# Kernel optimization log

Hardware: AMD Instinct MI355X
Metric: run time of the kernel (lower is better)

## Reference

```python
import jax, jax.numpy as jnp
import numpy as np

D, H, W, C = 24, 24, 16, 2        # image_dims + num_classes
THETA_ALPHA = 160.0               # bilateral spatial std
THETA_BETA = 3.0                  # bilateral intensity std
THETA_GAMMA = 3.0                 # spatial-only std
NUM_ITERATIONS = 5
N = D * H * W


def _gauss_kernel(feats):
    # Dense Gaussian kernel K_ij = exp(-0.5 * ||f_i - f_j||^2).
    # This is the exact filter that the permutohedral lattice approximates
    # (self-term included, matching the lattice splat/blur/slice behaviour).
    sq = jnp.sum(feats * feats, axis=-1)               # [N]
    d2 = sq[:, None] + sq[None, :] - 2.0 * feats @ feats.T
    return jnp.exp(-0.5 * jnp.maximum(d2, 0.0))        # [N, N]


def _positions():
    zz, yy, xx = jnp.meshgrid(jnp.arange(D), jnp.arange(H), jnp.arange(W), indexing='ij')
    return jnp.stack([zz, yy, xx], axis=-1).reshape(N, 3).astype(jnp.float32)


def setup_inputs() -> dict:
    key = jax.random.key(0)
    k1, k2 = jax.random.split(key)
    unaries = jax.random.normal(k1, (1, D, H, W, C), dtype=jnp.float32)
    rgb = jax.random.uniform(k2, (1, D, H, W, 1), dtype=jnp.float32)
    # learned params (build() initial values)
    spatial_ker_weights = jnp.array([1.41, 1.41], dtype=jnp.float32)
    bilateral_ker_weights = jnp.array([3.85, 3.85], dtype=jnp.float32)
    compatibility_matrix = jnp.eye(C, dtype=jnp.float32)
    return dict(unaries=unaries, rgb=rgb,
                spatial_ker_weights=spatial_ker_weights,
                bilateral_ker_weights=bilateral_ker_weights,
                compatibility_matrix=compatibility_matrix)


def reference(unaries, rgb, spatial_ker_weights, bilateral_ker_weights, compatibility_matrix):
    out_shape = unaries.shape
    u = unaries.reshape(N, C)                 # batch index 0 only, as in the TF code
    img = rgb.reshape(N, -1)
    pos = _positions()

    Ks = _gauss_kernel(pos / THETA_GAMMA)                                        # spatial kernel [N,N]
    Kb = _gauss_kernel(jnp.concatenate([pos / THETA_ALPHA, img / THETA_BETA], -1))  # bilateral kernel [N,N]

    # normalization = filter applied to all-ones (row sums)
    norm_s = jnp.sum(Ks, axis=-1, keepdims=True)   # [N,1]
    norm_b = jnp.sum(Kb, axis=-1, keepdims=True)   # [N,1]

    q = u
    for _ in range(NUM_ITERATIONS):
        spatial_out = (Ks @ q) / norm_s            # [N,C]
        bilateral_out = (Kb @ q) / norm_b          # [N,C]
        # diag(w_s) @ spatial.T + diag(w_b) @ bilateral.T  ==  per-class scaling
        message = spatial_out * spatial_ker_weights + bilateral_out * bilateral_ker_weights
        pairwise = message @ compatibility_matrix.T  # (compat @ msg.T).T
        q = u - pairwise
    return q.reshape(out_shape)
```

## Files before the change

kernel.cpp:

```cpp
#include <hip/hip_runtime.h>


#define DD 24
#define HH 24
#define WW 16
#define SLICE 384
#define NPTS 9216
#define NT 5
#define NFI 12
#define NFT 17
#define LOG2E 1.4426950408889634f
#define K3L   (LOG2E / 18.0f)
#define K160L (LOG2E / 51200.0f)

static __device__ __forceinline__ int iabs(int a) { return a < 0 ? -a : a; }

__global__ __launch_bounds__(SLICE)
void k_xy(const float2* __restrict__ qsrc, const float* __restrict__ rgb,
          float* __restrict__ tmp) {
    __shared__ float gk[32];
    __shared__ float sA[HH][WW + 1];
    __shared__ float sB[HH][WW + 1];
    const int z = blockIdx.x, f = blockIdx.y, t = threadIdx.x;
    const int y = t >> 4, x = t & 15;
    const int i = z * SLICE + t;

    const float kk = (f < 2) ? K3L : K160L;
    if (t < DD) gk[t] = exp2f(-(float)(t * t) * kk);

    float v;
    if (f < 2) {
        float2 q = qsrc[i];
        v = (f == 0) ? q.x : q.y;
    } else {
        float I3 = rgb[i] * (1.f / 3.f);
        float E = exp2f(-0.5f * LOG2E * I3 * I3);
        int k = (f < NFI) ? ((f - 2) >> 1) : (f - NFI);
        float P = E;
        for (int s = 0; s < k; ++s) P *= I3;
        if (f < NFI) {
            float2 q = qsrc[i];
            v = P * (((f - 2) & 1) ? q.y : q.x);
        } else {
            v = P;
        }
    }
    sA[y][x] = v;
    __syncthreads();

    float a = 0.f;
#pragma unroll
    for (int xp = 0; xp < WW; ++xp) a = fmaf(gk[iabs(x - xp)], sA[y][xp], a);
    sB[y][x] = a;
    __syncthreads();

    float b = 0.f;
#pragma unroll
    for (int yp = 0; yp < HH; ++yp) b = fmaf(gk[iabs(y - yp)], sB[yp][x], b);
    tmp[f * NPTS + i] = b;
}

__global__ __launch_bounds__(SLICE)
void k_zconv(const float* __restrict__ tmp, float* __restrict__ zout) {
    __shared__ float gk[32];
    const int z = blockIdx.x, f = blockIdx.y, t = threadIdx.x;
    const float kk = (f < 2) ? K3L : K160L;
    if (t < DD) gk[t] = exp2f(-(float)(t * t) * kk);
    __syncthreads();

    float acc = 0.f;
    const float* p = tmp + f * NPTS + t;
#pragma unroll 4
    for (int zp = 0; zp < DD; ++zp)
        acc = fmaf(gk[iabs(z - zp)], p[zp * SLICE], acc);
    zout[f * NPTS + z * SLICE + t] = acc;
}

__global__ __launch_bounds__(256)
void k_update(const float* __restrict__ zout, const float* __restrict__ rgb,
              const float2* __restrict__ u2,
              const float* __restrict__ sw, const float* __restrict__ bw,
              const float* __restrict__ compat,
              float* __restrict__ normb, float2* __restrict__ qnew,
              float2* __restrict__ out, int it) {
    __shared__ float g3s[32];
    const int t = threadIdx.x;
    const int i = blockIdx.x * 256 + t;
    if (t < DD) g3s[t] = exp2f(-(float)(t * t) * K3L);
    __syncthreads();

    const int z = i / SLICE;
    const int yx = i - z * SLICE;
    const int y = yx >> 4, x = yx & 15;

    float sx = 0.f, sy = 0.f, sz = 0.f;
#pragma unroll
    for (int xp = 0; xp < WW; ++xp) sx += g3s[iabs(x - xp)];
#pragma unroll
    for (int yp = 0; yp < HH; ++yp) sy += g3s[iabs(y - yp)];
#pragma unroll
    for (int zp = 0; zp < DD; ++zp) sz += g3s[iabs(z - zp)];
    const float inv_ns = 1.0f / (sx * sy * sz);

    const float I3 = rgb[i] * (1.f / 3.f);
    const float E = exp2f(-0.5f * LOG2E * I3 * I3);
    float Pt[NT];
    Pt[0] = E;
#pragma unroll
    for (int k = 1; k < NT; ++k) Pt[k] = Pt[k - 1] * I3;
    const float invf[NT] = {1.f, 1.f, 0.5f, 1.f / 6.f, 1.f / 24.f};

    float inv_nb;
    if (it == 0) {
        float nb = 0.f;
#pragma unroll
        for (int k = 0; k < NT; ++k)
            nb = fmaf(Pt[k] * invf[k], zout[(NFI + k) * NPTS + i], nb);
        normb[i] = nb;
        inv_nb = 1.0f / nb;
    } else {
        inv_nb = 1.0f / normb[i];
    }

    float b0 = 0.f, b1 = 0.f;
#pragma unroll
    for (int k = 0; k < NT; ++k) {
        float w = Pt[k] * invf[k];
        b0 = fmaf(w, zout[(2 + 2 * k) * NPTS + i], b0);
        b1 = fmaf(w, zout[(3 + 2 * k) * NPTS + i], b1);
    }
    b0 *= inv_nb;
    b1 *= inv_nb;

    float s0 = zout[i] * inv_ns;
    float s1 = zout[NPTS + i] * inv_ns;

    float m0 = s0 * sw[0] + b0 * bw[0];
    float m1 = s1 * sw[1] + b1 * bw[1];
    float p0 = fmaf(compat[0], m0, compat[1] * m1);
    float p1 = fmaf(compat[2], m0, compat[3] * m1);
    const float2 uu = u2[i];
    float2 qn = make_float2(uu.x - p0, uu.y - p1);
    qnew[i] = qn;
    if (it == 4) out[i] = qn;
}

extern "C" void kernel_launch(void* const* d_in, const int* in_sizes, int n_in,
                              void* d_out, int out_size, void* d_ws, size_t ws_size,
                              hipStream_t stream) {
    const float2* u2     = (const float2*)d_in[0];
    const float*  rgb    = (const float*)d_in[1];
    const float*  sw     = (const float*)d_in[2];
    const float*  bw     = (const float*)d_in[3];
    const float*  compat = (const float*)d_in[4];
    float2* out = (float2*)d_out;

    float* ws = (float*)d_ws;
    float*  tmp   = ws;
    float*  zout  = ws + NFT * NPTS;
    float*  normb = ws + 2 * NFT * NPTS;
    float2* qnew  = (float2*)(ws + 2 * NFT * NPTS + NPTS);

    k_xy<<<dim3(DD, NFT), SLICE, 0, stream>>>(u2, rgb, tmp);

    for (int it = 0; it < 5; ++it) {
        k_zconv<<<dim3(DD, it == 0 ? NFT : NFI), SLICE, 0, stream>>>(tmp, zout);
        k_update<<<NPTS / 256, 256, 0, stream>>>(zout, rgb, u2, sw, bw, compat,
                                                 normb, qnew, out, it);
        if (it < 4)
            k_xy<<<dim3(DD, NFI), SLICE, 0, stream>>>((const float2*)qnew, rgb, tmp);
    }
}
```

Baseline: 109.4 us.

## Fuse z-convolution, mean-field update and next xy-filter into one iteration kernel

After: 272.6 us. 149% more time.

```diff
diff --git a/kernel.cpp b/kernel.cpp
--- a/kernel.cpp
+++ b/kernel.cpp
@@ -16,8 +16,8 @@
 static __device__ __forceinline__ int iabs(int a) { return a < 0 ? -a : a; }
 
 __global__ __launch_bounds__(SLICE)
-void k_xy(const float2* __restrict__ qsrc, const float* __restrict__ rgb,
-          float* __restrict__ tmp) {
+void k_pre(const float2* __restrict__ u2, const float* __restrict__ rgb,
+           float* __restrict__ tmpA, float* __restrict__ tmpN) {
     __shared__ float gk[32];
     __shared__ float sA[HH][WW + 1];
     __shared__ float sB[HH][WW + 1];
@@ -30,7 +30,7 @@
 
     float v;
     if (f < 2) {
-        float2 q = qsrc[i];
+        float2 q = u2[i];
         v = (f == 0) ? q.x : q.y;
     } else {
         float I3 = rgb[i] * (1.f / 3.f);
@@ -39,7 +39,7 @@
         float P = E;
         for (int s = 0; s < k; ++s) P *= I3;
         if (f < NFI) {
-            float2 q = qsrc[i];
+            float2 q = u2[i];
             v = P * (((f - 2) & 1) ? q.y : q.x);
         } else {
             v = P;
@@ -57,42 +57,16 @@
     float b = 0.f;
 #pragma unroll
     for (int yp = 0; yp < HH; ++yp) b = fmaf(gk[iabs(y - yp)], sB[yp][x], b);
-    tmp[f * NPTS + i] = b;
-}
-
-__global__ __launch_bounds__(SLICE)
-void k_zconv(const float* __restrict__ tmp, float* __restrict__ zout) {
-    __shared__ float gk[32];
-    const int z = blockIdx.x, f = blockIdx.y, t = threadIdx.x;
-    const float kk = (f < 2) ? K3L : K160L;
-    if (t < DD) gk[t] = exp2f(-(float)(t * t) * kk);
-    __syncthreads();
-
-    float acc = 0.f;
-    const float* p = tmp + f * NPTS + t;
-#pragma unroll 4
-    for (int zp = 0; zp < DD; ++zp)
-        acc = fmaf(gk[iabs(z - zp)], p[zp * SLICE], acc);
-    zout[f * NPTS + z * SLICE + t] = acc;
-}
-
-__global__ __launch_bounds__(256)
-void k_update(const float* __restrict__ zout, const float* __restrict__ rgb,
-              const float2* __restrict__ u2,
-              const float* __restrict__ sw, const float* __restrict__ bw,
-              const float* __restrict__ compat,
-              float* __restrict__ normb, float2* __restrict__ qnew,
-              float2* __restrict__ out, int it) {
-    __shared__ float g3s[32];
-    const int t = threadIdx.x;
-    const int i = blockIdx.x * 256 + t;
-    if (t < DD) g3s[t] = exp2f(-(float)(t * t) * K3L);
-    __syncthreads();
-
-    const int z = i / SLICE;
-    const int yx = i - z * SLICE;
-    const int y = yx >> 4, x = yx & 15;
-
+    float* dst = (f < NFI) ? (tmpA + f * NPTS) : (tmpN + (f - NFI) * NPTS);
+    dst[i] = b;
+}
+
+static __device__ __forceinline__ void mf_update(
+        const float acc[12], const float* g3s, const float* Pt,
+        float inv_nb, int y, int x, int z,
+        const float* sw, const float* bw, const float* compat,
+        const float2 uu, float* q0o, float* q1o) {
+    const float invf[NT] = {1.f, 1.f, 0.5f, 1.f / 6.f, 1.f / 24.f};
     float sx = 0.f, sy = 0.f, sz = 0.f;
 #pragma unroll
     for (int xp = 0; xp < WW; ++xp) sx += g3s[iabs(x - xp)];
@@ -101,6 +75,60 @@
 #pragma unroll
     for (int zp = 0; zp < DD; ++zp) sz += g3s[iabs(z - zp)];
     const float inv_ns = 1.0f / (sx * sy * sz);
+
+    float b0 = 0.f, b1 = 0.f;
+#pragma unroll
+    for (int k = 0; k < NT; ++k) {
+        float w = Pt[k] * invf[k];
+        b0 = fmaf(w, acc[2 + 2 * k], b0);
+        b1 = fmaf(w, acc[3 + 2 * k], b1);
+    }
+    b0 *= inv_nb;
+    b1 *= inv_nb;
+    float s0 = acc[0] * inv_ns;
+    float s1 = acc[1] * inv_ns;
+    float m0 = s0 * sw[0] + b0 * bw[0];
+    float m1 = s1 * sw[1] + b1 * bw[1];
+    float p0 = fmaf(compat[0], m0, compat[1] * m1);
+    float p1 = fmaf(compat[2], m0, compat[3] * m1);
+    *q0o = uu.x - p0;
+    *q1o = uu.y - p1;
+}
+
+__global__ __launch_bounds__(SLICE)
+void k_iter(const float* __restrict__ tsrc, float* __restrict__ tdst,
+            const float* __restrict__ tmpN, const float* __restrict__ rgb,
+            const float2* __restrict__ u2,
+            const float* __restrict__ sw, const float* __restrict__ bw,
+            const float* __restrict__ compat,
+            float* __restrict__ normb, int it) {
+    __shared__ float g3s[32];
+    __shared__ float g160s[32];
+    __shared__ float2 cA[HH][WW + 1];
+    __shared__ float2 cB[HH][WW + 1];
+    const int z = blockIdx.x, g = blockIdx.y, t = threadIdx.x;
+    const int y = t >> 4, x = t & 15;
+    const int i = z * SLICE + t;
+
+    if (t < DD) {
+        g3s[t] = exp2f(-(float)(t * t) * K3L);
+        g160s[t] = exp2f(-(float)(t * t) * K160L);
+    }
+    __syncthreads();
+
+    float acc[12];
+#pragma unroll
+    for (int f = 0; f < 12; ++f) acc[f] = 0.f;
+    for (int zp = 0; zp < DD; ++zp) {
+        int d = iabs(z - zp);
+        float w3 = g3s[d], wb = g160s[d];
+        const float* base = tsrc + zp * SLICE + t;
+        acc[0] = fmaf(w3, base[0], acc[0]);
+        acc[1] = fmaf(w3, base[NPTS], acc[1]);
+#pragma unroll
+        for (int f = 2; f < 12; ++f)
+            acc[f] = fmaf(wb, base[f * NPTS], acc[f]);
+    }
 
     const float I3 = rgb[i] * (1.f / 3.f);
     const float E = exp2f(-0.5f * LOG2E * I3 * I3);
@@ -108,41 +136,105 @@
     Pt[0] = E;
 #pragma unroll
     for (int k = 1; k < NT; ++k) Pt[k] = Pt[k - 1] * I3;
-    const float invf[NT] = {1.f, 1.f, 0.5f, 1.f / 6.f, 1.f / 24.f};
 
     float inv_nb;
     if (it == 0) {
+        const float invf[NT] = {1.f, 1.f, 0.5f, 1.f / 6.f, 1.f / 24.f};
+        float accN[NT] = {0.f, 0.f, 0.f, 0.f, 0.f};
+        for (int zp = 0; zp < DD; ++zp) {
+            float wb = g160s[iabs(z - zp)];
+            const float* base = tmpN + zp * SLICE + t;
+#pragma unroll
+            for (int k = 0; k < NT; ++k)
+                accN[k] = fmaf(wb, base[k * NPTS], accN[k]);
+        }
         float nb = 0.f;
 #pragma unroll
-        for (int k = 0; k < NT; ++k)
-            nb = fmaf(Pt[k] * invf[k], zout[(NFI + k) * NPTS + i], nb);
-        normb[i] = nb;
+        for (int k = 0; k < NT; ++k) nb = fmaf(Pt[k] * invf[k], accN[k], nb);
+        if (g == 0) normb[i] = nb;
         inv_nb = 1.0f / nb;
     } else {
         inv_nb = 1.0f / normb[i];
     }
 
+    float q0, q1;
+    mf_update(acc, g3s, Pt, inv_nb, y, x, z, sw, bw, compat, u2[i], &q0, &q1);
+
+    float2 v;
+    const float* gk;
+    if (g == 0) { v = make_float2(q0, q1); gk = g3s; }
+    else        { float P = Pt[g - 1]; v = make_float2(P * q0, P * q1); gk = g160s; }
+
+    cA[y][x] = v;
+    __syncthreads();
+    float a0 = 0.f, a1 = 0.f;
+#pragma unroll
+    for (int xp = 0; xp < WW; ++xp) {
+        float w = gk[iabs(x - xp)];
+        float2 vv = cA[y][xp];
+        a0 = fmaf(w, vv.x, a0);
+        a1 = fmaf(w, vv.y, a1);
+    }
+    cB[y][x] = make_float2(a0, a1);
+    __syncthreads();
     float b0 = 0.f, b1 = 0.f;
 #pragma unroll
-    for (int k = 0; k < NT; ++k) {
-        float w = Pt[k] * invf[k];
-        b0 = fmaf(w, zout[(2 + 2 * k) * NPTS + i], b0);
-        b1 = fmaf(w, zout[(3 + 2 * k) * NPTS + i], b1);
-    }
-    b0 *= inv_nb;
-    b1 *= inv_nb;
-
-    float s0 = zout[i] * inv_ns;
-    float s1 = zout[NPTS + i] * inv_ns;
-
-    float m0 = s0 * sw[0] + b0 * bw[0];
-    float m1 = s1 * sw[1] + b1 * bw[1];
-    float p0 = fmaf(compat[0], m0, compat[1] * m1);
-    float p1 = fmaf(compat[2], m0, compat[3] * m1);
-    const float2 uu = u2[i];
-    float2 qn = make_float2(uu.x - p0, uu.y - p1);
-    qnew[i] = qn;
-    if (it == 4) out[i] = qn;
+    for (int yp = 0; yp < HH; ++yp) {
+        float w = gk[iabs(y - yp)];
+        float2 vv = cB[yp][x];
+        b0 = fmaf(w, vv.x, b0);
+        b1 = fmaf(w, vv.y, b1);
+    }
+    tdst[(2 * g) * NPTS + i] = b0;
+    tdst[(2 * g + 1) * NPTS + i] = b1;
+}
+
+__global__ __launch_bounds__(128)
+void k_final(const float* __restrict__ tsrc, const float* __restrict__ rgb,
+             const float2* __restrict__ u2,
+             const float* __restrict__ sw, const float* __restrict__ bw,
+             const float* __restrict__ compat,
+             const float* __restrict__ normb, float2* __restrict__ out) {
+    __shared__ float g3s[32];
+    __shared__ float g160s[32];
+    const int t = threadIdx.x;
+    const int i = blockIdx.x * 128 + t;
+    const int z = i / SLICE;
+    const int yx = i - z * SLICE;
+    const int y = yx >> 4, x = yx & 15;
+    const int col = yx;
+
+    if (t < DD) {
+        g3s[t] = exp2f(-(float)(t * t) * K3L);
+        g160s[t] = exp2f(-(float)(t * t) * K160L);
+    }
+    __syncthreads();
+
+    float acc[12];
+#pragma unroll
+    for (int f = 0; f < 12; ++f) acc[f] = 0.f;
+    for (int zp = 0; zp < DD; ++zp) {
+        int d = iabs(z - zp);
+        float w3 = g3s[d], wb = g160s[d];
+        const float* base = tsrc + zp * SLICE + col;
+        acc[0] = fmaf(w3, base[0], acc[0]);
+        acc[1] = fmaf(w3, base[NPTS], acc[1]);
+#pragma unroll
+        for (int f = 2; f < 12; ++f)
+            acc[f] = fmaf(wb, base[f * NPTS], acc[f]);
+    }
+
+    const float I3 = rgb[i] * (1.f / 3.f);
+    const float E = exp2f(-0.5f * LOG2E * I3 * I3);
+    float Pt[NT];
+    Pt[0] = E;
+#pragma unroll
+    for (int k = 1; k < NT; ++k) Pt[k] = Pt[k - 1] * I3;
+
+    float q0, q1;
+    mf_update(acc, g3s, Pt, 1.0f / normb[i], y, x, z, sw, bw, compat,
+              u2[i], &q0, &q1);
+    out[i] = make_float2(q0, q1);
 }
 
 extern "C" void kernel_launch(void* const* d_in, const int* in_sizes, int n_in,
@@ -156,18 +248,22 @@
     float2* out = (float2*)d_out;
 
     float* ws = (float*)d_ws;
-    float*  tmp   = ws;
-    float*  zout  = ws + NFT * NPTS;
-    float*  normb = ws + 2 * NFT * NPTS;
-    float2* qnew  = (float2*)(ws + 2 * NFT * NPTS + NPTS);
-
-    k_xy<<<dim3(DD, NFT), SLICE, 0, stream>>>(u2, rgb, tmp);
-
-    for (int it = 0; it < 5; ++it) {
-        k_zconv<<<dim3(DD, it == 0 ? NFT : NFI), SLICE, 0, stream>>>(tmp, zout);
-        k_update<<<NPTS / 256, 256, 0, stream>>>(zout, rgb, u2, sw, bw, compat,
-                                                 normb, qnew, out, it);
-        if (it < 4)
-            k_xy<<<dim3(DD, NFI), SLICE, 0, stream>>>((const float2*)qnew, rgb, tmp);
-    }
-}
+    float* tmpA  = ws;
+    float* tmpB  = ws + NFI * NPTS;
+    float* tmpN  = ws + 2 * NFI * NPTS;
+    float* normb = ws + (2 * NFI + NT) * NPTS;
+
+    k_pre<<<dim3(DD, NFT), SLICE, 0, stream>>>(u2, rgb, tmpA, tmpN);
+
+    const float* tsrc = tmpA;
+    float* tdst = tmpB;
+    for (int it = 0; it < 4; ++it) {
+        k_iter<<<dim3(DD, 6), SLICE, 0, stream>>>(tsrc, tdst, tmpN, rgb, u2,
+                                                  sw, bw, compat, normb, it);
+        const float* ns = tdst;
+        tdst = (float*)tsrc;
+        tsrc = ns;
+    }
+    k_final<<<NPTS / 128, 128, 0, stream>>>(tsrc, rgb, u2, sw, bw, compat,
+                                            normb, out);
+}
```

## Fuse mean-field update into xy-blur kernel to remove per-iteration launches

Applied to the files above, without the earlier changes.

After: 103.8 us. -5.1%, faster.

```diff
diff --git a/kernel.cpp b/kernel.cpp
--- a/kernel.cpp
+++ b/kernel.cpp
@@ -16,8 +16,8 @@
 static __device__ __forceinline__ int iabs(int a) { return a < 0 ? -a : a; }
 
 __global__ __launch_bounds__(SLICE)
-void k_xy(const float2* __restrict__ qsrc, const float* __restrict__ rgb,
-          float* __restrict__ tmp) {
+void k_pre(const float2* __restrict__ u2, const float* __restrict__ rgb,
+           float* __restrict__ tmp) {
     __shared__ float gk[32];
     __shared__ float sA[HH][WW + 1];
     __shared__ float sB[HH][WW + 1];
@@ -30,7 +30,7 @@
 
     float v;
     if (f < 2) {
-        float2 q = qsrc[i];
+        float2 q = u2[i];
         v = (f == 0) ? q.x : q.y;
     } else {
         float I3 = rgb[i] * (1.f / 3.f);
@@ -39,7 +39,7 @@
         float P = E;
         for (int s = 0; s < k; ++s) P *= I3;
         if (f < NFI) {
-            float2 q = qsrc[i];
+            float2 q = u2[i];
             v = P * (((f - 2) & 1) ? q.y : q.x);
         } else {
             v = P;
@@ -76,13 +76,114 @@
     zout[f * NPTS + z * SLICE + t] = acc;
 }
 
+static __device__ __forceinline__ void mf_update(
+        const float acc[12], const float* g3s, const float* Pt,
+        float inv_nb, int y, int x, int z,
+        const float* sw, const float* bw, const float* compat,
+        const float2 uu, float* q0o, float* q1o) {
+    const float invf[NT] = {1.f, 1.f, 0.5f, 1.f / 6.f, 1.f / 24.f};
+    float sx = 0.f, sy = 0.f, sz = 0.f;
+#pragma unroll
+    for (int xp = 0; xp < WW; ++xp) sx += g3s[iabs(x - xp)];
+#pragma unroll
+    for (int yp = 0; yp < HH; ++yp) sy += g3s[iabs(y - yp)];
+#pragma unroll
+    for (int zp = 0; zp < DD; ++zp) sz += g3s[iabs(z - zp)];
+    const float inv_ns = 1.0f / (sx * sy * sz);
+
+    float b0 = 0.f, b1 = 0.f;
+#pragma unroll
+    for (int k = 0; k < NT; ++k) {
+        float w = Pt[k] * invf[k];
+        b0 = fmaf(w, acc[2 + 2 * k], b0);
+        b1 = fmaf(w, acc[3 + 2 * k], b1);
+    }
+    b0 *= inv_nb;
+    b1 *= inv_nb;
+    float s0 = acc[0] * inv_ns;
+    float s1 = acc[1] * inv_ns;
+    float m0 = s0 * sw[0] + b0 * bw[0];
+    float m1 = s1 * sw[1] + b1 * bw[1];
+    float p0 = fmaf(compat[0], m0, compat[1] * m1);
+    float p1 = fmaf(compat[2], m0, compat[3] * m1);
+    *q0o = uu.x - p0;
+    *q1o = uu.y - p1;
+}
+
+__global__ __launch_bounds__(SLICE)
+void k_xyupd(const float* __restrict__ zout, const float* __restrict__ rgb,
+             const float2* __restrict__ u2,
+             const float* __restrict__ sw, const float* __restrict__ bw,
+             const float* __restrict__ compat,
+             float* __restrict__ normb, float* __restrict__ tmp, int it) {
+    __shared__ float g3s[32];
+    __shared__ float gk[32];
+    __shared__ float sA[HH][WW + 1];
+    __shared__ float sB[HH][WW + 1];
+    const int z = blockIdx.x, f = blockIdx.y, t = threadIdx.x;
+    const int y = t >> 4, x = t & 15;
+    const int i = z * SLICE + t;
+
+    if (t < DD) {
+        g3s[t] = exp2f(-(float)(t * t) * K3L);
+        gk[t] = exp2f(-(float)(t * t) * ((f < 2) ? K3L : K160L));
+    }
+    __syncthreads();
+
+    float acc[12];
+#pragma unroll
+    for (int k = 0; k < 12; ++k) acc[k] = zout[k * NPTS + i];
+
+    const float I3 = rgb[i] * (1.f / 3.f);
+    const float E = exp2f(-0.5f * LOG2E * I3 * I3);
+    float Pt[NT];
+    Pt[0] = E;
+#pragma unroll
+    for (int k = 1; k < NT; ++k) Pt[k] = Pt[k - 1] * I3;
+
+    float inv_nb;
+    if (it == 0) {
+        const float invf[NT] = {1.f, 1.f, 0.5f, 1.f / 6.f, 1.f / 24.f};
+        float nb = 0.f;
+#pragma unroll
+        for (int k = 0; k < NT; ++k)
+            nb = fmaf(Pt[k] * invf[k], zout[(NFI + k) * NPTS + i], nb);
+        if (f == 0) normb[i] = nb;
+        inv_nb = 1.0f / nb;
+    } else {
+        inv_nb = 1.0f / normb[i];
+    }
+
+    float q0, q1;
+    mf_update(acc, g3s, Pt, inv_nb, y, x, z, sw, bw, compat, u2[i], &q0, &q1);
+
+    float v;
+    if (f == 0) v = q0;
+    else if (f == 1) v = q1;
+    else {
+        int k = (f - 2) >> 1;
+        v = Pt[k] * (((f - 2) & 1) ? q1 : q0);
+    }
+
+    sA[y][x] = v;
+    __syncthreads();
+    float a = 0.f;
+#pragma unroll
+    for (int xp = 0; xp < WW; ++xp) a = fmaf(gk[iabs(x - xp)], sA[y][xp], a);
+    sB[y][x] = a;
+    __syncthreads();
+    float b = 0.f;
+#pragma unroll
+    for (int yp = 0; yp < HH; ++yp) b = fmaf(gk[iabs(y - yp)], sB[yp][x], b);
+    tmp[f * NPTS + i] = b;
+}
+
 __global__ __launch_bounds__(256)
-void k_update(const float* __restrict__ zout, const float* __restrict__ rgb,
-              const float2* __restrict__ u2,
-              const float* __restrict__ sw, const float* __restrict__ bw,
-              const float* __restrict__ compat,
-              float* __restrict__ normb, float2* __restrict__ qnew,
-              float2* __restrict__ out, int it) {
+void k_final(const float* __restrict__ zout, const float* __restrict__ rgb,
+             const float2* __restrict__ u2,
+             const float* __restrict__ sw, const float* __restrict__ bw,
+             const float* __restrict__ compat,
+             const float* __restrict__ normb, float2* __restrict__ out) {
     __shared__ float g3s[32];
     const int t = threadIdx.x;
     const int i = blockIdx.x * 256 + t;
@@ -93,14 +194,9 @@
     const int yx = i - z * SLICE;
     const int y = yx >> 4, x = yx & 15;
 
-    float sx = 0.f, sy = 0.f, sz = 0.f;
-#pragma unroll
-    for (int xp = 0; xp < WW; ++xp) sx += g3s[iabs(x - xp)];
-#pragma unroll
-    for (int yp = 0; yp < HH; ++yp) sy += g3s[iabs(y - yp)];
-#pragma unroll
-    for (int zp = 0; zp < DD; ++zp) sz += g3s[iabs(z - zp)];
-    const float inv_ns = 1.0f / (sx * sy * sz);
+    float acc[12];
+#pragma unroll
+    for (int k = 0; k < 12; ++k) acc[k] = zout[k * NPTS + i];
 
     const float I3 = rgb[i] * (1.f / 3.f);
     const float E = exp2f(-0.5f * LOG2E * I3 * I3);
@@ -108,41 +204,11 @@
     Pt[0] = E;
 #pragma unroll
     for (int k = 1; k < NT; ++k) Pt[k] = Pt[k - 1] * I3;
-    const float invf[NT] = {1.f, 1.f, 0.5f, 1.f / 6.f, 1.f / 24.f};
-
-    float inv_nb;
-    if (it == 0) {
-        float nb = 0.f;
-#pragma unroll
-        for (int k = 0; k < NT; ++k)
-            nb = fmaf(Pt[k] * invf[k], zout[(NFI + k) * NPTS + i], nb);
-        normb[i] = nb;
-        inv_nb = 1.0f / nb;
-    } else {
-        inv_nb = 1.0f / normb[i];
-    }
-
-    float b0 = 0.f, b1 = 0.f;
-#pragma unroll
-    for (int k = 0; k < NT; ++k) {
-        float w = Pt[k] * invf[k];
-        b0 = fmaf(w, zout[(2 + 2 * k) * NPTS + i], b0);
-        b1 = fmaf(w, zout[(3 + 2 * k) * NPTS + i], b1);
-    }
-    b0 *= inv_nb;
-    b1 *= inv_nb;
-
-    float s0 = zout[i] * inv_ns;
-    float s1 = zout[NPTS + i] * inv_ns;
-
-    float m0 = s0 * sw[0] + b0 * bw[0];
-    float m1 = s1 * sw[1] + b1 * bw[1];
-    float p0 = fmaf(compat[0], m0, compat[1] * m1);
-    float p1 = fmaf(compat[2], m0, compat[3] * m1);
-    const float2 uu = u2[i];
-    float2 qn = make_float2(uu.x - p0, uu.y - p1);
-    qnew[i] = qn;
-    if (it == 4) out[i] = qn;
+
+    float q0, q1;
+    mf_update(acc, g3s, Pt, 1.0f / normb[i], y, x, z, sw, bw, compat,
+              u2[i], &q0, &q1);
+    out[i] = make_float2(q0, q1);
 }
 
 extern "C" void kernel_launch(void* const* d_in, const int* in_sizes, int n_in,
@@ -156,18 +222,19 @@
     float2* out = (float2*)d_out;
 
     float* ws = (float*)d_ws;
-    float*  tmp   = ws;
-    float*  zout  = ws + NFT * NPTS;
-    float*  normb = ws + 2 * NFT * NPTS;
-    float2* qnew  = (float2*)(ws + 2 * NFT * NPTS + NPTS);
-
-    k_xy<<<dim3(DD, NFT), SLICE, 0, stream>>>(u2, rgb, tmp);
+    float* tmp   = ws;
+    float* zout  = ws + NFT * NPTS;
+    float* normb = ws + 2 * NFT * NPTS;
+
+    k_pre<<<dim3(DD, NFT), SLICE, 0, stream>>>(u2, rgb, tmp);
 
     for (int it = 0; it < 5; ++it) {
         k_zconv<<<dim3(DD, it == 0 ? NFT : NFI), SLICE, 0, stream>>>(tmp, zout);
-        k_update<<<NPTS / 256, 256, 0, stream>>>(zout, rgb, u2, sw, bw, compat,
-                                                 normb, qnew, out, it);
         if (it < 4)
-            k_xy<<<dim3(DD, NFI), SLICE, 0, stream>>>((const float2*)qnew, rgb, tmp);
-    }
-}
+            k_xyupd<<<dim3(DD, NFI), SLICE, 0, stream>>>(zout, rgb, u2, sw, bw,
+                                                         compat, normb, tmp, it);
+        else
+            k_final<<<NPTS / 256, 256, 0, stream>>>(zout, rgb, u2, sw, bw,
+                                                    compat, normb, out);
+    }
+}
```
